# Kernel optimization log

Measured on AMD Instinct MI355X. Metric: run time of the kernel, lower is better.

Reference implementation:

```python
import jax, jax.numpy as jnp
import numpy as np

EPS = 1e-5

def setup_inputs() -> dict:
    key = jax.random.key(0)
    ks = jax.random.split(key, 12)
    N, d0, d1, d2, qh, qo = 8192, 128, 256, 256, 128, 1
    state = jax.random.normal(ks[0], (N, d0), dtype=jnp.float32)
    adjacent_matrix = jax.random.uniform(ks[1], (N, N), dtype=jnp.float32)
    s = 0.05
    return {
        "state": state,
        "adjacent_matrix": adjacent_matrix,
        "gamma": jnp.ones((d0,), jnp.float32),
        "beta": jnp.zeros((d0,), jnp.float32),
        "W1": jax.random.normal(ks[2], (d0, d1), jnp.float32) * s,
        "b1": jnp.zeros((d1,), jnp.float32),
        "W2": jax.random.normal(ks[3], (d1, d2), jnp.float32) * s,
        "b2": jnp.zeros((d2,), jnp.float32),
        "Wq1": jax.random.normal(ks[4], (d2, qh), jnp.float32) * s,
        "bq1": jnp.zeros((qh,), jnp.float32),
        "Wq2": jax.random.normal(ks[5], (qh, qo), jnp.float32) * s,
        "bq2": jnp.zeros((qo,), jnp.float32),
    }


def reference(state, adjacent_matrix, gamma, beta, W1, b1, W2, b2, Wq1, bq1, Wq2, bq2):
    # LinkBatchNorm: BatchNorm1d over node (batch) axis, training-mode statistics
    mean = jnp.mean(state, axis=0)
    var = jnp.var(state, axis=0)
    x = (state - mean) * jax.lax.rsqrt(var + EPS) * gamma + beta  # [N, d0]
    # GraphCNN: two layers of relu(A @ X @ W + b)
    h = jax.nn.relu(adjacent_matrix @ (x @ W1) + b1)   # [N, d1]
    h = jax.nn.relu(adjacent_matrix @ (h @ W2) + b2)   # [N, d2]
    # QNetwork: per-node MLP -> Q value
    q = jax.nn.relu(h @ Wq1 + bq1) @ Wq2 + bq2         # [N, 1]
    return q
```

## Files before the change

kernel.cpp:

```cpp
#include <hip/hip_runtime.h>
#include <stdint.h>

#define NN 8192
#define D0 128
#define D1 256
#define D2 256
#define QH 128
#define EPSV 1e-5f

using bf16x8 = __attribute__((ext_vector_type(8))) __bf16;
using f32x4  = __attribute__((ext_vector_type(4))) float;

__device__ __forceinline__ unsigned short f2bf(float f) {
    union { float f; unsigned int u; } v; v.f = f;
    unsigned int r = v.u + 0x7FFFu + ((v.u >> 16) & 1u);
    return (unsigned short)(r >> 16);
}
__device__ __forceinline__ float bf2f(unsigned short h) {
    union { unsigned int u; float f; } v; v.u = ((unsigned int)h) << 16;
    return v.f;
}
__device__ __forceinline__ void async_ld16(const void* g, void* l) {
    __builtin_amdgcn_global_load_lds(
        (__attribute__((address_space(1))) void*)(g),
        (__attribute__((address_space(3))) void*)(l), 16, 0, 0);
}

__global__ __launch_bounds__(256) void k_castA(const float* __restrict__ A,
                                               unsigned short* __restrict__ Abf,
                                               float* __restrict__ rs) {
    __shared__ float sred[256];
    int t = threadIdx.x;
    size_t row = blockIdx.x;
    const float* ap = A + row * NN;
    unsigned short* op = Abf + row * NN;
    float s = 0.f;
#pragma unroll
    for (int i = 0; i < 8; ++i) {
        int c = i * 1024 + t * 4;
        float4 v = *(const float4*)(ap + c);
        s += v.x + v.y + v.z + v.w;
        ushort4 o; o.x = f2bf(v.x); o.y = f2bf(v.y); o.z = f2bf(v.z); o.w = f2bf(v.w);
        *(ushort4*)(op + c) = o;
    }
    sred[t] = s;
    __syncthreads();
    if (t < 128) sred[t] += sred[t + 128];
    __syncthreads();
    if (t < 64) {
        float v = sred[t] + sred[t + 64];
#pragma unroll
        for (int d = 32; d > 0; d >>= 1) v += __shfl_down(v, d, 64);
        if (t == 0) rs[row] = v;
    }
}

__global__ void k_stats(const float* __restrict__ state,
                        float* __restrict__ psum, float* __restrict__ psq,
                        float* __restrict__ acc4k) {
    int j = threadIdx.x;
    int b = blockIdx.x;
    int gid = b * 128 + j;
    if (gid < 1024) acc4k[gid] = 0.f;
    const float* p = state + (size_t)b * 32 * D0 + j;
    float s = 0.f, sq = 0.f;
#pragma unroll 4
    for (int r = 0; r < 32; ++r) { float x = p[(size_t)r * D0]; s += x; sq += x * x; }
    psum[b * D0 + j] = s;
    psq [b * D0 + j] = sq;
}

__global__ void k_finalize(const float* __restrict__ psum, const float* __restrict__ psq,
                           const float* __restrict__ gamma, const float* __restrict__ beta,
                           const float* __restrict__ W1,
                           float* __restrict__ scale, float* __restrict__ shift,
                           float* __restrict__ c1) {
    __shared__ float s_shift[D0];
    int t = threadIdx.x;
    if (t < D0) {
        float s = 0.f, sq = 0.f;
        for (int b = 0; b < 256; ++b) { s += psum[b * D0 + t]; sq += psq[b * D0 + t]; }
        float mean = s * (1.0f / NN);
        float var  = sq * (1.0f / NN) - mean * mean;
        float sc = gamma[t] * rsqrtf(var + EPSV);
        float sh = beta[t] - mean * sc;
        scale[t] = sc; shift[t] = sh; s_shift[t] = sh;
    }
    __syncthreads();
    float acc = 0.f;
    for (int k = 0; k < D0; ++k) acc += s_shift[k] * W1[(size_t)k * D1 + t];
    c1[t] = acc;
}

__global__ void k_prep_weights(const float* __restrict__ W1, const float* __restrict__ W2,
                               const float* __restrict__ scale,
                               unsigned short* __restrict__ W1st,
                               unsigned short* __restrict__ W2t) {
    int idx = blockIdx.x * 256 + threadIdx.x;
    if (idx < 32768) {
        int n = idx >> 7, k = idx & 127;
        W1st[idx] = f2bf(W1[(size_t)k * D1 + n] * scale[k]);
    } else {
        int i = idx - 32768; int n = i >> 8, k = i & 255;
        W2t[i] = f2bf(W2[(size_t)k * D2 + n]);
    }
}

template <int N, int K, bool A_FP32, bool BIAS>
__global__ __launch_bounds__(256, 4) void k_small_gemm(
        const void* __restrict__ Aptr, const unsigned short* __restrict__ Bt,
        const float* __restrict__ bias, unsigned short* __restrict__ out) {
    constexpr int WN = N / 4;
    constexpr int NJ = WN / 16;
    constexpr int BI = N / 64;
    __shared__ unsigned short Alds[32 * 32];
    __shared__ unsigned short Blds[N * 32];
    int t = threadIdx.x, lane = t & 63, w = t >> 6;
    int m0 = blockIdx.x * 32;
    int lr = lane & 15, lk = (lane >> 4) * 8;
    int wc = w * WN;
    f32x4 acc[2][NJ] = {};

    for (int kk = 0; kk < K; kk += 32) {
        __syncthreads();
        if constexpr (A_FP32) {
            const float* A = (const float*)Aptr;
            int row = t >> 3, kc = (t & 7) * 4;
            float4 v = *(const float4*)(A + (size_t)(m0 + row) * K + kk + kc);
            uint2 p;
            p.x = ((unsigned)f2bf(v.y) << 16) | f2bf(v.x);
            p.y = ((unsigned)f2bf(v.w) << 16) | f2bf(v.z);
            *(uint2*)&Alds[row * 32 + kc] = p;
        } else {
            if (w < 2) {
                const unsigned short* A = (const unsigned short*)Aptr;
                int row = w * 16 + (lane >> 2);
                async_ld16(A + (size_t)(m0 + row) * K + kk + (lane & 3) * 8, &Alds[w * 512]);
            }
        }
#pragma unroll
        for (int i = 0; i < BI; ++i) {
            int n = w * WN + i * 16 + (lane >> 2);
            async_ld16(Bt + (size_t)n * K + kk + (lane & 3) * 8, &Blds[(w * WN + i * 16) * 32]);
        }
        __syncthreads();
        bf16x8 a[2], b[NJ];
#pragma unroll
        for (int i = 0; i < 2; ++i) a[i] = *(const bf16x8*)&Alds[(i * 16 + lr) * 32 + lk];
#pragma unroll
        for (int j = 0; j < NJ; ++j) b[j] = *(const bf16x8*)&Blds[(wc + j * 16 + lr) * 32 + lk];
#pragma unroll
        for (int i = 0; i < 2; ++i)
#pragma unroll
            for (int j = 0; j < NJ; ++j)
                acc[i][j] = __builtin_amdgcn_mfma_f32_16x16x32_bf16(a[i], b[j], acc[i][j], 0, 0, 0);
    }
    int q = lane >> 4;
#pragma unroll
    for (int j = 0; j < NJ; ++j) {
        int n = wc + j * 16 + lr;
        float bv = 0.f;
        if constexpr (BIAS) bv = bias[n];
#pragma unroll
        for (int i = 0; i < 2; ++i) {
#pragma unroll
            for (int r = 0; r < 4; ++r) {
                int m = m0 + i * 16 + q * 4 + r;
                out[(size_t)m * N + n] = f2bf(acc[i][j][r] + bv);
            }
        }
    }
}

__global__ void k_transpose(const unsigned short* __restrict__ in, unsigned short* __restrict__ out,
                            float* __restrict__ colsum) {
    __shared__ unsigned short tile[64 * 68];
    __shared__ float cp[4][64];
    int t = threadIdx.x;
    int r0 = blockIdx.x * 64, c0 = blockIdx.y * 64;
#pragma unroll
    for (int p = 0; p < 4; ++p) {
        int row = (t >> 4) + p * 16, col = (t & 15) * 4;
        *(ushort4*)&tile[row * 68 + col] = *(const ushort4*)&in[(size_t)(r0 + row) * 256 + c0 + col];
    }
    __syncthreads();
    int n = t >> 2;
#pragma unroll
    for (int s = 0; s < 2; ++s) {
        int mo = (t & 3) * 16 + s * 8;
        unsigned short v[8];
#pragma unroll
        for (int e = 0; e < 8; ++e) v[e] = tile[(mo + e) * 68 + n];
        *(uint4*)&out[(size_t)(c0 + n) * NN + r0 + mo] = *(const uint4*)v;
    }
    int col = t & 63, gg = t >> 6;
    float s = 0.f;
#pragma unroll
    for (int r = 0; r < 16; ++r) s += bf2f(tile[(gg * 16 + r) * 68 + col]);
    cp[gg][col] = s;
    __syncthreads();
    if (t < 64) atomicAdd(colsum + c0 + t, cp[0][t] + cp[1][t] + cp[2][t] + cp[3][t]);
}

__global__ __launch_bounds__(512, 4) void k_big_gemm5(
        const unsigned short* __restrict__ Abf, const unsigned short* __restrict__ Yt,
        float* __restrict__ Cp) {
    __shared__ unsigned short Alds[3][128 * 32];
    __shared__ unsigned short Blds[3][256 * 32];
    int t = threadIdx.x, lane = t & 63, w = t >> 6;
    int m0 = blockIdx.x * 128;
    int kbeg = blockIdx.y * 1024;
    int wr = (w & 1) * 64, wc = (w >> 1) * 64;
    int lr = lane & 15, q = lane >> 4;
    f32x4 acc[4][4] = {};

    int srow = lane >> 2;
    int hsw = (lane & 3) ^ ((srow ^ (srow >> 2)) & 3);
    const unsigned short* agp = Abf + (size_t)(m0 + w * 16 + srow) * NN + kbeg + hsw * 8;
    const unsigned short* bg0 = Yt + (size_t)(w * 32 + srow) * NN + kbeg + hsw * 8;
    const unsigned short* bg1 = Yt + (size_t)(w * 32 + 16 + srow) * NN + kbeg + hsw * 8;
    unsigned short* aL  = (unsigned short*)Alds + w * 512;
    unsigned short* bL0 = (unsigned short*)Blds + w * 1024;
    unsigned short* bL1 = bL0 + 512;
    int xsr = (lr ^ (lr >> 2)) & 3;
    int lks = ((q ^ xsr) & 3) * 8;

#pragma unroll
    for (int pt = 0; pt < 2; ++pt) {
        async_ld16(agp + pt * 32, aL  + pt * 4096);
        async_ld16(bg0 + pt * 32, bL0 + pt * 8192);
        async_ld16(bg1 + pt * 32, bL1 + pt * 8192);
    }
    asm volatile("s_waitcnt vmcnt(3)" ::: "memory");
    __builtin_amdgcn_s_barrier();
    __builtin_amdgcn_sched_barrier(0);

    int cur = 0;
#define GEMM5_COMPUTE(BUF)                                                              \
    {                                                                                   \
        const unsigned short* Ab = (const unsigned short*)Alds + (BUF) * 4096;          \
        const unsigned short* Bb = (const unsigned short*)Blds + (BUF) * 8192;          \
        bf16x8 a[4];                                                                    \
        _Pragma("unroll")                                                               \
        for (int i = 0; i < 4; ++i) a[i] = *(const bf16x8*)&Ab[(wr + i * 16 + lr) * 32 + lks]; \
        _Pragma("unroll")                                                               \
        for (int j = 0; j < 4; ++j) {                                                   \
            bf16x8 b = *(const bf16x8*)&Bb[(wc + j * 16 + lr) * 32 + lks];              \
            _Pragma("unroll")                                                           \
            for (int i = 0; i < 4; ++i)                                                 \
                acc[i][j] = __builtin_amdgcn_mfma_f32_16x16x32_bf16(a[i], b, acc[i][j], 0, 0, 0); \
        }                                                                               \
    }

#pragma unroll 3
    for (int it = 0; it < 30; ++it) {
        int nb = cur + 2; if (nb >= 3) nb -= 3;
        int ko = (it + 2) * 32;
        async_ld16(agp + ko, aL  + nb * 4096);
        async_ld16(bg0 + ko, bL0 + nb * 8192);
        async_ld16(bg1 + ko, bL1 + nb * 8192);
        GEMM5_COMPUTE(cur)
        asm volatile("s_waitcnt vmcnt(3)" ::: "memory");
        __builtin_amdgcn_s_barrier();
        __builtin_amdgcn_sched_barrier(0);
        ++cur; if (cur >= 3) cur = 0;
    }
    GEMM5_COMPUTE(cur)
    asm volatile("s_waitcnt vmcnt(0)" ::: "memory");
    __builtin_amdgcn_s_barrier();
    __builtin_amdgcn_sched_barrier(0);
    ++cur; if (cur >= 3) cur = 0;
    GEMM5_COMPUTE(cur)
#undef GEMM5_COMPUTE

    float* outp = Cp + (size_t)blockIdx.y * NN * 256;
#pragma unroll
    for (int i = 0; i < 4; ++i)
#pragma unroll
        for (int j = 0; j < 4; ++j) {
            int n = wc + j * 16 + lr;
#pragma unroll
            for (int r = 0; r < 4; ++r) {
                int m = m0 + wr + i * 16 + q * 4 + r;
                outp[(size_t)m * 256 + n] = acc[i][j][r];
            }
        }
}

__global__ void k_s2(const float* __restrict__ colB, const float* __restrict__ colH1,
                     const float* __restrict__ W2, float* __restrict__ s2) {
    int n = threadIdx.x;
    float acc = 0.f;
    for (int k = 0; k < 256; ++k) acc += colH1[k] * W2[(size_t)k * 256 + n];
    s2[n] = colB[n] - acc;
}

__global__ __launch_bounds__(256) void k_reduce8(
        const float* __restrict__ Cp, const float* __restrict__ rsA,
        const float* __restrict__ bias, const float* __restrict__ sn,
        unsigned short* __restrict__ out, float* __restrict__ colH1) {
    __shared__ float rs_s[16];
    __shared__ float cs[4][256];
    int t = threadIdx.x;
    int m0 = blockIdx.x * 16;
    const size_t S = (size_t)NN * 256;
    if (t < 16) rs_s[t] = rsA[m0 + t] * (1.0f / 8192.0f);
    __syncthreads();
    int g = t >> 6, cq = (t & 63) * 4;
    float4 snv = *(const float4*)(sn + cq);
    float4 bv  = *(const float4*)(bias + cq);
    float c0 = 0.f, c1a = 0.f, c2 = 0.f, c3 = 0.f;
#pragma unroll
    for (int r4 = 0; r4 < 4; ++r4) {
        int row = g * 4 + r4;
        size_t base = (size_t)(m0 + row) * 256 + cq;
        float4 a = {0.f, 0.f, 0.f, 0.f};
#pragma unroll
        for (int s = 0; s < 8; ++s) {
            float4 p = *(const float4*)(Cp + (size_t)s * S + base);
            a.x += p.x; a.y += p.y; a.z += p.z; a.w += p.w;
        }
        float rsv = rs_s[row];
        float x0 = fmaxf(a.x + bv.x - rsv * snv.x, 0.f);
        float x1 = fmaxf(a.y + bv.y - rsv * snv.y, 0.f);
        float x2 = fmaxf(a.z + bv.z - rsv * snv.z, 0.f);
        float x3 = fmaxf(a.w + bv.w - rsv * snv.w, 0.f);
        ushort4 o; o.x = f2bf(x0); o.y = f2bf(x1); o.z = f2bf(x2); o.w = f2bf(x3);
        *(ushort4*)(out + base) = o;
        c0 += x0; c1a += x1; c2 += x2; c3 += x3;
    }
    cs[g][cq] = c0; cs[g][cq + 1] = c1a; cs[g][cq + 2] = c2; cs[g][cq + 3] = c3;
    __syncthreads();
    float tot = cs[0][t] + cs[1][t] + cs[2][t] + cs[3][t];
    atomicAdd(colH1 + t, tot);
}

__global__ __launch_bounds__(256) void k_reduce_qhead(
        const float* __restrict__ Cp, const float* __restrict__ rsA,
        const float* __restrict__ bias, const float* __restrict__ sn,
        const float* __restrict__ Wq1, const float* __restrict__ bq1,
        const float* __restrict__ Wq2, const float* __restrict__ bq2,
        float* __restrict__ out) {
    __shared__ float sh[16][256];
    __shared__ float rs_s[16];
    __shared__ float red[4][8];
    int t = threadIdx.x;
    int m0 = blockIdx.x * 16;
    const size_t S = (size_t)NN * 256;
    if (t < 16) rs_s[t] = rsA[m0 + t] * (1.0f / 8192.0f);
    __syncthreads();
    int g = t >> 6, cq = (t & 63) * 4;
    float4 snv = *(const float4*)(sn + cq);
    float4 bv  = *(const float4*)(bias + cq);
#pragma unroll
    for (int r4 = 0; r4 < 4; ++r4) {
        int row = g * 4 + r4;
        size_t base = (size_t)(m0 + row) * 256 + cq;
        float4 a = {0.f, 0.f, 0.f, 0.f};
#pragma unroll
        for (int s = 0; s < 8; ++s) {
            float4 p = *(const float4*)(Cp + (size_t)s * S + base);
            a.x += p.x; a.y += p.y; a.z += p.z; a.w += p.w;
        }
        float rsv = rs_s[row];
        float4 o;
        o.x = fmaxf(a.x + bv.x - rsv * snv.x, 0.f);
        o.y = fmaxf(a.y + bv.y - rsv * snv.y, 0.f);
        o.z = fmaxf(a.z + bv.z - rsv * snv.z, 0.f);
        o.w = fmaxf(a.w + bv.w - rsv * snv.w, 0.f);
        *(float4*)&sh[row][cq] = o;
    }
    __syncthreads();
    int h = t & 127, rg = t >> 7;
    float acc[8] = {};
    const float* wq = Wq1 + h;
    for (int n4 = 0; n4 < 64; ++n4) {
        int n = n4 * 4;
        float wa = wq[(size_t)(n + 0) * QH];
        float wb = wq[(size_t)(n + 1) * QH];
        float wcc = wq[(size_t)(n + 2) * QH];
        float wd = wq[(size_t)(n + 3) * QH];
#pragma unroll
        for (int r = 0; r < 8; ++r) {
            float4 sv = *(const float4*)&sh[rg * 8 + r][n];
            acc[r] = fmaf(sv.x, wa, fmaf(sv.y, wb, fmaf(sv.z, wcc, fmaf(sv.w, wd, acc[r]))));
        }
    }
    float b1v = bq1[h], w2v = Wq2[h];
    int wid = t >> 6, lane = t & 63;
#pragma unroll
    for (int r = 0; r < 8; ++r) {
        float v = fmaxf(acc[r] + b1v, 0.f) * w2v;
#pragma unroll
        for (int d = 32; d > 0; d >>= 1) v += __shfl_down(v, d, 64);
        if (lane == 0) red[wid][r] = v;
    }
    __syncthreads();
    if (t < 16) {
        int rg2 = t >> 3, r = t & 7;
        out[m0 + rg2 * 8 + r] = red[rg2 * 2][r] + red[rg2 * 2 + 1][r] + bq2[0];
    }
}

extern "C" void kernel_launch(void* const* d_in, const int* in_sizes, int n_in,
                              void* d_out, int out_size, void* d_ws, size_t ws_size,
                              hipStream_t stream) {
    const float* state = (const float*)d_in[0];
    const float* adj   = (const float*)d_in[1];
    const float* gamma = (const float*)d_in[2];
    const float* beta  = (const float*)d_in[3];
    const float* W1    = (const float*)d_in[4];
    const float* b1    = (const float*)d_in[5];
    const float* W2    = (const float*)d_in[6];
    const float* b2    = (const float*)d_in[7];
    const float* Wq1   = (const float*)d_in[8];
    const float* bq1   = (const float*)d_in[9];
    const float* Wq2   = (const float*)d_in[10];
    const float* bq2   = (const float*)d_in[11];
    float* out = (float*)d_out;

    char* ws = (char*)d_ws;
    float* psum  = (float*)(ws + 0);
    float* psq   = (float*)(ws + 131072);
    float* scale = (float*)(ws + 262144);
    float* shift = (float*)(ws + 262656);
    float* c1    = (float*)(ws + 263168);
    float* colA  = (float*)(ws + 264192);
    float* colB  = (float*)(ws + 265216);
    float* colH1 = (float*)(ws + 266240);
    float* s2    = (float*)(ws + 267264);
    unsigned short* W1st = (unsigned short*)(ws + 268288);
    unsigned short* W2t  = (unsigned short*)(ws + 333824);
    unsigned short* Ybuf = (unsigned short*)(ws + (size_t)1  * (1u << 20));
    unsigned short* Ytb  = (unsigned short*)(ws + (size_t)5  * (1u << 20));
    unsigned short* Hbuf = (unsigned short*)(ws + (size_t)9  * (1u << 20));
    float*          rsA  = (float*)(ws + (size_t)14 * (1u << 20));
    float*          Cp   = (float*)(ws + (size_t)22 * (1u << 20));
    unsigned short* Abf  = (unsigned short*)(ws + (size_t)128 * (1u << 20));

    k_castA<<<8192, 256, 0, stream>>>(adj, Abf, rsA);
    k_stats<<<256, 128, 0, stream>>>(state, psum, psq, colA);
    k_finalize<<<1, 256, 0, stream>>>(psum, psq, gamma, beta, W1, scale, shift, c1);
    k_prep_weights<<<384, 256, 0, stream>>>(W1, W2, scale, W1st, W2t);

    k_small_gemm<256, 128, true, true><<<256, 256, 0, stream>>>(state, W1st, c1, Ybuf);
    k_transpose<<<dim3(128, 4), 256, 0, stream>>>(Ybuf, Ytb, colA);
    k_big_gemm5<<<dim3(64, 8), 512, 0, stream>>>(Abf, Ytb, Cp);
    k_reduce8<<<512, 256, 0, stream>>>(Cp, rsA, b1, colA, Hbuf, colH1);

    k_small_gemm<256, 256, false, false><<<256, 256, 0, stream>>>(Hbuf, W2t, nullptr, Ybuf);
    k_transpose<<<dim3(128, 4), 256, 0, stream>>>(Ybuf, Ytb, colB);
    k_s2<<<1, 256, 0, stream>>>(colB, colH1, W2, s2);
    k_big_gemm5<<<dim3(64, 8), 512, 0, stream>>>(Abf, Ytb, Cp);
    k_reduce_qhead<<<512, 256, 0, stream>>>(Cp, rsA, b2, s2, Wq1, bq1, Wq2, bq2, out);
}
```

Before: 599.1 us.

## Fuse fp32-to-bf16 adjacency cast and row sums into first big GEMM

Removes the separate pass that casts the fp32 adjacency matrix to bf16 and computes its row sums. The first big GEMM now loads fp32 A tiles into registers, packs them to bf16 with a hardware pack instruction, writes them both to LDS and to the global bf16 copy for the second GEMM, and accumulates row sums with atomics. This saves one full read of the 256MB matrix, at the cost of register-staged A loads in the GEMM main loop instead of direct async loads to LDS, which may reduce its overlap.

```diff
diff --git a/kernel.cpp b/kernel.cpp
--- a/kernel.cpp
+++ b/kernel.cpp
@@ -20,47 +20,24 @@
     union { unsigned int u; float f; } v; v.u = ((unsigned int)h) << 16;
     return v.f;
 }
+__device__ __forceinline__ unsigned pkbf(float a, float b) {
+    unsigned r;
+    asm("v_cvt_pk_bf16_f32 %0, %1, %2" : "=v"(r) : "v"(a), "v"(b));
+    return r;
+}
 __device__ __forceinline__ void async_ld16(const void* g, void* l) {
     __builtin_amdgcn_global_load_lds(
         (__attribute__((address_space(1))) void*)(g),
         (__attribute__((address_space(3))) void*)(l), 16, 0, 0);
 }
 
-__global__ __launch_bounds__(256) void k_castA(const float* __restrict__ A,
-                                               unsigned short* __restrict__ Abf,
-                                               float* __restrict__ rs) {
-    __shared__ float sred[256];
-    int t = threadIdx.x;
-    size_t row = blockIdx.x;
-    const float* ap = A + row * NN;
-    unsigned short* op = Abf + row * NN;
-    float s = 0.f;
-#pragma unroll
-    for (int i = 0; i < 8; ++i) {
-        int c = i * 1024 + t * 4;
-        float4 v = *(const float4*)(ap + c);
-        s += v.x + v.y + v.z + v.w;
-        ushort4 o; o.x = f2bf(v.x); o.y = f2bf(v.y); o.z = f2bf(v.z); o.w = f2bf(v.w);
-        *(ushort4*)(op + c) = o;
-    }
-    sred[t] = s;
-    __syncthreads();
-    if (t < 128) sred[t] += sred[t + 128];
-    __syncthreads();
-    if (t < 64) {
-        float v = sred[t] + sred[t + 64];
-#pragma unroll
-        for (int d = 32; d > 0; d >>= 1) v += __shfl_down(v, d, 64);
-        if (t == 0) rs[row] = v;
-    }
-}
-
 __global__ void k_stats(const float* __restrict__ state,
                         float* __restrict__ psum, float* __restrict__ psq,
-                        float* __restrict__ acc4k) {
+                        float* __restrict__ acc4k, float* __restrict__ rsA) {
     int j = threadIdx.x;
     int b = blockIdx.x;
     int gid = b * 128 + j;
+    if (gid < 8192) rsA[gid] = 0.f;
     if (gid < 1024) acc4k[gid] = 0.f;
     const float* p = state + (size_t)b * 32 * D0 + j;
     float s = 0.f, sq = 0.f;
@@ -202,6 +179,127 @@
     if (t < 64) atomicAdd(colsum + c0 + t, cp[0][t] + cp[1][t] + cp[2][t] + cp[3][t]);
 }
 
+__global__ __launch_bounds__(512, 4) void k_big_gemm6(
+        const float* __restrict__ A, const unsigned short* __restrict__ Yt,
+        float* __restrict__ Cp, unsigned short* __restrict__ Abf,
+        float* __restrict__ rsA) {
+    __shared__ unsigned short Alds[3][128 * 32];
+    __shared__ unsigned short Blds[3][256 * 32];
+    int t = threadIdx.x, lane = t & 63, w = t >> 6;
+    int m0 = blockIdx.x * 128;
+    int kbeg = blockIdx.y * 1024;
+    int wr = (w & 1) * 64, wc = (w >> 1) * 64;
+    int lr = lane & 15, q = lane >> 4;
+    f32x4 acc[4][4] = {};
+
+    int arow = t >> 2, aseg = t & 3;
+    int axs = (arow ^ (arow >> 2)) & 3;
+    const float* agp = A + (size_t)(m0 + arow) * NN + kbeg + aseg * 8;
+    unsigned short* abfp = Abf + (size_t)(m0 + arow) * NN + kbeg + aseg * 8;
+    int awr = arow * 32 + ((aseg ^ axs) & 3) * 8;
+
+    int srow = lane >> 2;
+    int hsw = (lane & 3) ^ ((srow ^ (srow >> 2)) & 3);
+    const unsigned short* bg0 = Yt + (size_t)(w * 32 + srow) * NN + kbeg + hsw * 8;
+    const unsigned short* bg1 = Yt + (size_t)(w * 32 + 16 + srow) * NN + kbeg + hsw * 8;
+    unsigned short* ALf = &Alds[0][0];
+    unsigned short* bL0 = &Blds[0][0] + w * 1024;
+    unsigned short* bL1 = bL0 + 512;
+
+    int xsr = (lr ^ (lr >> 2)) & 3;
+    int lks = ((q ^ xsr) & 3) * 8;
+
+    float rs = 0.f;
+    float4 p0a, p0b, p1a, p1b;
+
+#define G6_COMPUTE(BUF)                                                                  \
+    {                                                                                    \
+        const unsigned short* Ab = ALf + (BUF) * 4096;                                   \
+        const unsigned short* Bb = &Blds[0][0] + (BUF) * 8192;                           \
+        bf16x8 a[4];                                                                     \
+        _Pragma("unroll")                                                                \
+        for (int i = 0; i < 4; ++i) a[i] = *(const bf16x8*)&Ab[(wr + i * 16 + lr) * 32 + lks]; \
+        _Pragma("unroll")                                                                \
+        for (int j = 0; j < 4; ++j) {                                                    \
+            bf16x8 b = *(const bf16x8*)&Bb[(wc + j * 16 + lr) * 32 + lks];               \
+            _Pragma("unroll")                                                            \
+            for (int i = 0; i < 4; ++i)                                                  \
+                acc[i][j] = __builtin_amdgcn_mfma_f32_16x16x32_bf16(a[i], b, acc[i][j], 0, 0, 0); \
+        }                                                                                \
+    }
+
+#define G6_WRITE(WB, KOFF, pWa, pWb)                                                     \
+    {                                                                                    \
+        uint4 u = { pkbf(pWa.x, pWa.y), pkbf(pWa.z, pWa.w),                              \
+                    pkbf(pWb.x, pWb.y), pkbf(pWb.z, pWb.w) };                            \
+        *(uint4*)&ALf[(WB) * 4096 + awr] = u;                                            \
+        *(uint4*)(abfp + (KOFF)) = u;                                                    \
+        rs += pWa.x + pWa.y + pWa.z + pWa.w + pWb.x + pWb.y + pWb.z + pWb.w;             \
+    }
+
+    p0a = *(const float4*)(agp);      p0b = *(const float4*)(agp + 4);
+    async_ld16(bg0, bL0);             async_ld16(bg1, bL1);
+    p1a = *(const float4*)(agp + 32); p1b = *(const float4*)(agp + 36);
+    async_ld16(bg0 + 32, bL0 + 8192); async_ld16(bg1 + 32, bL1 + 8192);
+    asm volatile("s_waitcnt vmcnt(4)" ::: "memory");
+    G6_WRITE(0, 0, p0a, p0b)
+    asm volatile("s_waitcnt lgkmcnt(0)" ::: "memory");
+    __builtin_amdgcn_s_barrier();
+    __builtin_amdgcn_sched_barrier(0);
+
+#define G6_STEP(S, pLa, pLb, pWa, pWb)                                                   \
+    {                                                                                    \
+        constexpr int CURb = (S) % 3, NBb = ((S) + 2) % 3, WBb = ((S) + 1) % 3;          \
+        int ko = base + ((S) + 2) * 32;                                                  \
+        pLa = *(const float4*)(agp + ko);                                                \
+        pLb = *(const float4*)(agp + ko + 4);                                            \
+        async_ld16(bg0 + ko, bL0 + NBb * 8192);                                          \
+        async_ld16(bg1 + ko, bL1 + NBb * 8192);                                          \
+        G6_COMPUTE(CURb)                                                                 \
+        asm volatile("s_waitcnt vmcnt(5)" ::: "memory");                                 \
+        G6_WRITE(WBb, base + ((S) + 1) * 32, pWa, pWb)                                   \
+        asm volatile("s_waitcnt lgkmcnt(0)" ::: "memory");                               \
+        __builtin_amdgcn_s_barrier();                                                    \
+        __builtin_amdgcn_sched_barrier(0);                                               \
+    }
+
+    for (int i6 = 0; i6 < 5; ++i6) {
+        int base = i6 * 192;
+        G6_STEP(0, p0a, p0b, p1a, p1b)
+        G6_STEP(1, p1a, p1b, p0a, p0b)
+        G6_STEP(2, p0a, p0b, p1a, p1b)
+        G6_STEP(3, p1a, p1b, p0a, p0b)
+        G6_STEP(4, p0a, p0b, p1a, p1b)
+        G6_STEP(5, p1a, p1b, p0a, p0b)
+    }
+    G6_COMPUTE(0)
+    asm volatile("s_waitcnt vmcnt(0)" ::: "memory");
+    G6_WRITE(1, 31 * 32, p1a, p1b)
+    asm volatile("s_waitcnt lgkmcnt(0)" ::: "memory");
+    __builtin_amdgcn_s_barrier();
+    __builtin_amdgcn_sched_barrier(0);
+    G6_COMPUTE(1)
+#undef G6_STEP
+#undef G6_WRITE
+#undef G6_COMPUTE
+
+    float* outp = Cp + (size_t)blockIdx.y * NN * 256;
+#pragma unroll
+    for (int i = 0; i < 4; ++i)
+#pragma unroll
+        for (int j = 0; j < 4; ++j) {
+            int n = wc + j * 16 + lr;
+#pragma unroll
+            for (int r = 0; r < 4; ++r) {
+                int m = m0 + wr + i * 16 + q * 4 + r;
+                outp[(size_t)m * 256 + n] = acc[i][j][r];
+            }
+        }
+    rs += __shfl_xor(rs, 1, 64);
+    rs += __shfl_xor(rs, 2, 64);
+    if ((lane & 3) == 0) atomicAdd(rsA + m0 + arow, rs);
+}
+
 __global__ __launch_bounds__(512, 4) void k_big_gemm5(
         const unsigned short* __restrict__ Abf, const unsigned short* __restrict__ Yt,
         float* __restrict__ Cp) {
@@ -219,8 +317,8 @@
     const unsigned short* agp = Abf + (size_t)(m0 + w * 16 + srow) * NN + kbeg + hsw * 8;
     const unsigned short* bg0 = Yt + (size_t)(w * 32 + srow) * NN + kbeg + hsw * 8;
     const unsigned short* bg1 = Yt + (size_t)(w * 32 + 16 + srow) * NN + kbeg + hsw * 8;
-    unsigned short* aL  = (unsigned short*)Alds + w * 512;
-    unsigned short* bL0 = (unsigned short*)Blds + w * 1024;
+    unsigned short* aL  = &Alds[0][0] + w * 512;
+    unsigned short* bL0 = &Blds[0][0] + w * 1024;
     unsigned short* bL1 = bL0 + 512;
     int xsr = (lr ^ (lr >> 2)) & 3;
     int lks = ((q ^ xsr) & 3) * 8;
@@ -238,8 +336,8 @@
     int cur = 0;
 #define GEMM5_COMPUTE(BUF)                                                              \
     {                                                                                   \
-        const unsigned short* Ab = (const unsigned short*)Alds + (BUF) * 4096;          \
-        const unsigned short* Bb = (const unsigned short*)Blds + (BUF) * 8192;          \
+        const unsigned short* Ab = &Alds[0][0] + (BUF) * 4096;                          \
+        const unsigned short* Bb = &Blds[0][0] + (BUF) * 8192;                          \
         bf16x8 a[4];                                                                    \
         _Pragma("unroll")                                                               \
         for (int i = 0; i < 4; ++i) a[i] = *(const bf16x8*)&Ab[(wr + i * 16 + lr) * 32 + lks]; \
@@ -438,14 +536,13 @@
     float*          Cp   = (float*)(ws + (size_t)22 * (1u << 20));
     unsigned short* Abf  = (unsigned short*)(ws + (size_t)128 * (1u << 20));
 
-    k_castA<<<8192, 256, 0, stream>>>(adj, Abf, rsA);
-    k_stats<<<256, 128, 0, stream>>>(state, psum, psq, colA);
+    k_stats<<<256, 128, 0, stream>>>(state, psum, psq, colA, rsA);
     k_finalize<<<1, 256, 0, stream>>>(psum, psq, gamma, beta, W1, scale, shift, c1);
     k_prep_weights<<<384, 256, 0, stream>>>(W1, W2, scale, W1st, W2t);
 
     k_small_gemm<256, 128, true, true><<<256, 256, 0, stream>>>(state, W1st, c1, Ybuf);
     k_transpose<<<dim3(128, 4), 256, 0, stream>>>(Ybuf, Ytb, colA);
-    k_big_gemm5<<<dim3(64, 8), 512, 0, stream>>>(Abf, Ytb, Cp);
+    k_big_gemm6<<<dim3(64, 8), 512, 0, stream>>>(adj, Ytb, Cp, Abf, rsA);
     k_reduce8<<<512, 256, 0, stream>>>(Cp, rsA, b1, colA, Hbuf, colH1);
 
     k_small_gemm<256, 256, false, false><<<256, 256, 0, stream>>>(Hbuf, W2t, nullptr, Ybuf);
```

Result: slower. 728.1 us (+21.5%).

## Store bf16 adjacency and Y in K-tiled panel layout for contiguous GEMM loads

Applied to the files above, without the earlier changes.

Replaces the row-major bf16 cast of the adjacency matrix with a cast that writes K-tiled panels ([K/32][N][32]), and likewise writes the transposed Y into K-panel layout. The big GEMM then reads each 32-wide K slab from one contiguous region instead of striding across rows of length 8192, which is meant to improve locality and TLB behaviour on the async global-to-LDS loads. The cast also uses packed hardware bf16 conversion and computes row sums through atomics, which needs rsA zeroed in k_stats. The risk is lower write coalescing in the cast kernel (64 blocks of 16-element runs) and the extra atomic traffic.

```diff
diff --git a/kernel.cpp b/kernel.cpp
--- a/kernel.cpp
+++ b/kernel.cpp
@@ -20,47 +20,24 @@
     union { unsigned int u; float f; } v; v.u = ((unsigned int)h) << 16;
     return v.f;
 }
+__device__ __forceinline__ unsigned pkbf(float a, float b) {
+    unsigned r;
+    asm("v_cvt_pk_bf16_f32 %0, %1, %2" : "=v"(r) : "v"(a), "v"(b));
+    return r;
+}
 __device__ __forceinline__ void async_ld16(const void* g, void* l) {
     __builtin_amdgcn_global_load_lds(
         (__attribute__((address_space(1))) void*)(g),
         (__attribute__((address_space(3))) void*)(l), 16, 0, 0);
 }
 
-__global__ __launch_bounds__(256) void k_castA(const float* __restrict__ A,
-                                               unsigned short* __restrict__ Abf,
-                                               float* __restrict__ rs) {
-    __shared__ float sred[256];
-    int t = threadIdx.x;
-    size_t row = blockIdx.x;
-    const float* ap = A + row * NN;
-    unsigned short* op = Abf + row * NN;
-    float s = 0.f;
-#pragma unroll
-    for (int i = 0; i < 8; ++i) {
-        int c = i * 1024 + t * 4;
-        float4 v = *(const float4*)(ap + c);
-        s += v.x + v.y + v.z + v.w;
-        ushort4 o; o.x = f2bf(v.x); o.y = f2bf(v.y); o.z = f2bf(v.z); o.w = f2bf(v.w);
-        *(ushort4*)(op + c) = o;
-    }
-    sred[t] = s;
-    __syncthreads();
-    if (t < 128) sred[t] += sred[t + 128];
-    __syncthreads();
-    if (t < 64) {
-        float v = sred[t] + sred[t + 64];
-#pragma unroll
-        for (int d = 32; d > 0; d >>= 1) v += __shfl_down(v, d, 64);
-        if (t == 0) rs[row] = v;
-    }
-}
-
 __global__ void k_stats(const float* __restrict__ state,
                         float* __restrict__ psum, float* __restrict__ psq,
-                        float* __restrict__ acc4k) {
+                        float* __restrict__ acc4k, float* __restrict__ rsA) {
     int j = threadIdx.x;
     int b = blockIdx.x;
     int gid = b * 128 + j;
+    if (gid < 8192) rsA[gid] = 0.f;
     if (gid < 1024) acc4k[gid] = 0.f;
     const float* p = state + (size_t)b * 32 * D0 + j;
     float s = 0.f, sq = 0.f;
@@ -104,6 +81,34 @@
         int i = idx - 32768; int n = i >> 8, k = i & 255;
         W2t[i] = f2bf(W2[(size_t)k * D2 + n]);
     }
+}
+
+__global__ __launch_bounds__(256) void k_castA_T(const float* __restrict__ A,
+                                                 unsigned short* __restrict__ AbfT,
+                                                 float* __restrict__ rs) {
+    int t = threadIdx.x;
+    int row = blockIdx.x * 128 + (t >> 1);
+    int off = (t & 1) * 16;
+    const float* ap = A + (size_t)row * NN + blockIdx.y * 2048 + off;
+    unsigned short* op = AbfT + (size_t)(blockIdx.y * 64) * ((size_t)NN * 32)
+                              + (size_t)row * 32 + off;
+    const size_t PL = (size_t)NN * 32;
+    float s = 0.f;
+    for (int kt = 0; kt < 64; ++kt) {
+        const float* p = ap + kt * 32;
+        float4 v0 = *(const float4*)(p);
+        float4 v1 = *(const float4*)(p + 4);
+        float4 v2 = *(const float4*)(p + 8);
+        float4 v3 = *(const float4*)(p + 12);
+        s += v0.x + v0.y + v0.z + v0.w + v1.x + v1.y + v1.z + v1.w
+           + v2.x + v2.y + v2.z + v2.w + v3.x + v3.y + v3.z + v3.w;
+        uint4 u0 = { pkbf(v0.x, v0.y), pkbf(v0.z, v0.w), pkbf(v1.x, v1.y), pkbf(v1.z, v1.w) };
+        uint4 u1 = { pkbf(v2.x, v2.y), pkbf(v2.z, v2.w), pkbf(v3.x, v3.y), pkbf(v3.z, v3.w) };
+        *(uint4*)(op + (size_t)kt * PL) = u0;
+        *(uint4*)(op + (size_t)kt * PL + 8) = u1;
+    }
+    s += __shfl_xor(s, 1, 64);
+    if ((t & 1) == 0) atomicAdd(rs + row, s);
 }
 
 template <int N, int K, bool A_FP32, bool BIAS>
@@ -191,7 +196,8 @@
         unsigned short v[8];
 #pragma unroll
         for (int e = 0; e < 8; ++e) v[e] = tile[(mo + e) * 68 + n];
-        *(uint4*)&out[(size_t)(c0 + n) * NN + r0 + mo] = *(const uint4*)v;
+        int kt = (r0 + mo) >> 5;
+        *(uint4*)&out[(size_t)kt * 8192 + (c0 + n) * 32 + (mo & 31)] = *(const uint4*)v;
     }
     int col = t & 63, gg = t >> 6;
     float s = 0.f;
@@ -202,44 +208,46 @@
     if (t < 64) atomicAdd(colsum + c0 + t, cp[0][t] + cp[1][t] + cp[2][t] + cp[3][t]);
 }
 
-__global__ __launch_bounds__(512, 4) void k_big_gemm5(
-        const unsigned short* __restrict__ Abf, const unsigned short* __restrict__ Yt,
+__global__ __launch_bounds__(512, 4) void k_big_gemm7(
+        const unsigned short* __restrict__ AbfT, const unsigned short* __restrict__ Ytb,
         float* __restrict__ Cp) {
     __shared__ unsigned short Alds[3][128 * 32];
     __shared__ unsigned short Blds[3][256 * 32];
     int t = threadIdx.x, lane = t & 63, w = t >> 6;
     int m0 = blockIdx.x * 128;
-    int kbeg = blockIdx.y * 1024;
+    int kt0 = blockIdx.y * 32;
     int wr = (w & 1) * 64, wc = (w >> 1) * 64;
     int lr = lane & 15, q = lane >> 4;
     f32x4 acc[4][4] = {};
 
+    const size_t AS = (size_t)NN * 32;
+    const int    BS = 256 * 32;
     int srow = lane >> 2;
     int hsw = (lane & 3) ^ ((srow ^ (srow >> 2)) & 3);
-    const unsigned short* agp = Abf + (size_t)(m0 + w * 16 + srow) * NN + kbeg + hsw * 8;
-    const unsigned short* bg0 = Yt + (size_t)(w * 32 + srow) * NN + kbeg + hsw * 8;
-    const unsigned short* bg1 = Yt + (size_t)(w * 32 + 16 + srow) * NN + kbeg + hsw * 8;
-    unsigned short* aL  = (unsigned short*)Alds + w * 512;
-    unsigned short* bL0 = (unsigned short*)Blds + w * 1024;
+    const unsigned short* agp = AbfT + (size_t)kt0 * AS + (size_t)(m0 + w * 16 + srow) * 32 + hsw * 8;
+    const unsigned short* bg0 = Ytb + (size_t)kt0 * BS + (w * 32 + srow) * 32 + hsw * 8;
+    const unsigned short* bg1 = bg0 + 16 * 32;
+    unsigned short* aL  = &Alds[0][0] + w * 512;
+    unsigned short* bL0 = &Blds[0][0] + w * 1024;
     unsigned short* bL1 = bL0 + 512;
     int xsr = (lr ^ (lr >> 2)) & 3;
     int lks = ((q ^ xsr) & 3) * 8;
 
 #pragma unroll
     for (int pt = 0; pt < 2; ++pt) {
-        async_ld16(agp + pt * 32, aL  + pt * 4096);
-        async_ld16(bg0 + pt * 32, bL0 + pt * 8192);
-        async_ld16(bg1 + pt * 32, bL1 + pt * 8192);
+        async_ld16(agp + (size_t)pt * AS, aL  + pt * 4096);
+        async_ld16(bg0 + (size_t)pt * BS, bL0 + pt * 8192);
+        async_ld16(bg1 + (size_t)pt * BS, bL1 + pt * 8192);
     }
     asm volatile("s_waitcnt vmcnt(3)" ::: "memory");
     __builtin_amdgcn_s_barrier();
     __builtin_amdgcn_sched_barrier(0);
 
     int cur = 0;
-#define GEMM5_COMPUTE(BUF)                                                              \
+#define GEMM7_COMPUTE(BUF)                                                              \
     {                                                                                   \
-        const unsigned short* Ab = (const unsigned short*)Alds + (BUF) * 4096;          \
-        const unsigned short* Bb = (const unsigned short*)Blds + (BUF) * 8192;          \
+        const unsigned short* Ab = &Alds[0][0] + (BUF) * 4096;                          \
+        const unsigned short* Bb = &Blds[0][0] + (BUF) * 8192;                          \
         bf16x8 a[4];                                                                    \
         _Pragma("unroll")                                                               \
         for (int i = 0; i < 4; ++i) a[i] = *(const bf16x8*)&Ab[(wr + i * 16 + lr) * 32 + lks]; \
@@ -255,23 +263,22 @@
 #pragma unroll 3
     for (int it = 0; it < 30; ++it) {
         int nb = cur + 2; if (nb >= 3) nb -= 3;
-        int ko = (it + 2) * 32;
-        async_ld16(agp + ko, aL  + nb * 4096);
-        async_ld16(bg0 + ko, bL0 + nb * 8192);
-        async_ld16(bg1 + ko, bL1 + nb * 8192);
-        GEMM5_COMPUTE(cur)
+        async_ld16(agp + (size_t)(it + 2) * AS, aL  + nb * 4096);
+        async_ld16(bg0 + (size_t)(it + 2) * BS, bL0 + nb * 8192);
+        async_ld16(bg1 + (size_t)(it + 2) * BS, bL1 + nb * 8192);
+        GEMM7_COMPUTE(cur)
         asm volatile("s_waitcnt vmcnt(3)" ::: "memory");
         __builtin_amdgcn_s_barrier();
         __builtin_amdgcn_sched_barrier(0);
         ++cur; if (cur >= 3) cur = 0;
     }
-    GEMM5_COMPUTE(cur)
+    GEMM7_COMPUTE(cur)
     asm volatile("s_waitcnt vmcnt(0)" ::: "memory");
     __builtin_amdgcn_s_barrier();
     __builtin_amdgcn_sched_barrier(0);
     ++cur; if (cur >= 3) cur = 0;
-    GEMM5_COMPUTE(cur)
-#undef GEMM5_COMPUTE
+    GEMM7_COMPUTE(cur)
+#undef GEMM7_COMPUTE
 
     float* outp = Cp + (size_t)blockIdx.y * NN * 256;
 #pragma unroll
@@ -436,21 +443,21 @@
     unsigned short* Hbuf = (unsigned short*)(ws + (size_t)9  * (1u << 20));
     float*          rsA  = (float*)(ws + (size_t)14 * (1u << 20));
     float*          Cp   = (float*)(ws + (size_t)22 * (1u << 20));
-    unsigned short* Abf  = (unsigned short*)(ws + (size_t)128 * (1u << 20));
-
-    k_castA<<<8192, 256, 0, stream>>>(adj, Abf, rsA);
-    k_stats<<<256, 128, 0, stream>>>(state, psum, psq, colA);
+    unsigned short* AbfT = (unsigned short*)(ws + (size_t)128 * (1u << 20));
+
+    k_stats<<<256, 128, 0, stream>>>(state, psum, psq, colA, rsA);
     k_finalize<<<1, 256, 0, stream>>>(psum, psq, gamma, beta, W1, scale, shift, c1);
     k_prep_weights<<<384, 256, 0, stream>>>(W1, W2, scale, W1st, W2t);
+    k_castA_T<<<dim3(64, 4), 256, 0, stream>>>(adj, AbfT, rsA);
 
     k_small_gemm<256, 128, true, true><<<256, 256, 0, stream>>>(state, W1st, c1, Ybuf);
     k_transpose<<<dim3(128, 4), 256, 0, stream>>>(Ybuf, Ytb, colA);
-    k_big_gemm5<<<dim3(64, 8), 512, 0, stream>>>(Abf, Ytb, Cp);
+    k_big_gemm7<<<dim3(64, 8), 512, 0, stream>>>(AbfT, Ytb, Cp);
     k_reduce8<<<512, 256, 0, stream>>>(Cp, rsA, b1, colA, Hbuf, colH1);
 
     k_small_gemm<256, 256, false, false><<<256, 256, 0, stream>>>(Hbuf, W2t, nullptr, Ybuf);
     k_transpose<<<dim3(128, 4), 256, 0, stream>>>(Ybuf, Ytb, colB);
     k_s2<<<1, 256, 0, stream>>>(colB, colH1, W2, s2);
-    k_big_gemm5<<<dim3(64, 8), 512, 0, stream>>>(Abf, Ytb, Cp);
+    k_big_gemm7<<<dim3(64, 8), 512, 0, stream>>>(AbfT, Ytb, Cp);
     k_reduce_qhead<<<512, 256, 0, stream>>>(Cp, rsA, b2, s2, Wq1, bq1, Wq2, bq2, out);
 }
```

Measured after the change: 613.7 us. 1.02x slower.
